# Optimization experiments

Hardware: AMD Instinct MI355X
Metric: run time of the kernel (lower is better)

The kernel has to match this reference:

```python
import jax, jax.numpy as jnp
import numpy as np

TEMPERATURE = 0.07
NEG = -1e9  # stand-in for -inf on the diagonal; exp(NEG) == 0


def setup_inputs() -> dict:
    key = jax.random.key(0)
    k1, k2, k3 = jax.random.split(key, 3)
    B, D = 4096, 1024
    return {
        "anchor_features": jax.random.normal(k1, (B, D), dtype=jnp.float32),
        "positive_features": jax.random.normal(k2, (B, D), dtype=jnp.float32),
        "labels": jax.random.randint(k3, (B,), 0, 2),
    }


def reference(anchor_features, positive_features, labels):
    B = anchor_features.shape[0]
    # L2-normalize (normalize=True)
    a = anchor_features / jnp.linalg.norm(anchor_features, axis=1, keepdims=True)
    p = positive_features / jnp.linalg.norm(positive_features, axis=1, keepdims=True)
    feats = jnp.concatenate([a, p], axis=0)                      # [2B, D]
    sim = jnp.matmul(feats, feats.T) / TEMPERATURE               # [2B, 2B]
    diag = jnp.eye(2 * B, dtype=bool)
    sim = jnp.where(diag, NEG, sim)                              # mask self-similarity
    # logsumexp over all non-self entries per row (diag contributes exp(NEG)=0)
    lse = jax.nn.logsumexp(sim, axis=1)                          # [2B]
    # positive pair similarity: sim[i, i+B] == sim[i+B, i] == <a_i, p_i>/t
    cross = jnp.sum(a * p, axis=1) / TEMPERATURE                 # [B]
    pos_sim = jnp.concatenate([cross, cross])                    # [2B]
    lab = jnp.concatenate([labels, labels]).astype(sim.dtype)    # [2B], 0/1
    per_row = (-pos_sim + lse) * lab
    num_pos = jnp.sum(lab)
    return jnp.where(num_pos > 0, jnp.sum(per_row) / num_pos, jnp.float32(0.0))
```

## Files before the change

### kernel.cpp

```cpp
#include <hip/hip_runtime.h>
#include <hip/hip_bf16.h>

#define TEMP_INV (1.0f / 0.07f)
#define LOG2E 1.4426950408889634f
#define LN2 0.6931471805599453f
#define CFIX 21.0f

typedef __attribute__((ext_vector_type(4))) float f32x4;

__device__ __forceinline__ void gload16(const unsigned char* g,
                                        unsigned char* l) {
  __builtin_amdgcn_global_load_lds(
      (const __attribute__((address_space(1))) void*)g,
      (__attribute__((address_space(3))) void*)l, 16, 0, 0);
}

__global__ __launch_bounds__(256) void norm_kernel(
    const float* __restrict__ A, const float* __restrict__ P,
    unsigned char* __restrict__ F, float* __restrict__ cross,
    float* __restrict__ lsum, int B, int D) {
  const int row = blockIdx.x;
  const int t = threadIdx.x;
  {
    const int zi = row * 256 + t;
    if (zi < 2 * B) lsum[zi] = 0.f;
  }
  const float4* a4 = reinterpret_cast<const float4*>(A + (size_t)row * D);
  const float4* p4 = reinterpret_cast<const float4*>(P + (size_t)row * D);
  const int n4 = D >> 2;
  float sa = 0.f, sp = 0.f, sx = 0.f;
  for (int i = t; i < n4; i += 256) {
    float4 av = a4[i], pv = p4[i];
    sa += av.x * av.x + av.y * av.y + av.z * av.z + av.w * av.w;
    sp += pv.x * pv.x + pv.y * pv.y + pv.z * pv.z + pv.w * pv.w;
    sx += av.x * pv.x + av.y * pv.y + av.z * pv.z + av.w * pv.w;
  }
#pragma unroll
  for (int off = 32; off; off >>= 1) {
    sa += __shfl_down(sa, off);
    sp += __shfl_down(sp, off);
    sx += __shfl_down(sx, off);
  }
  __shared__ float red[3][4];
  const int wid = t >> 6, lane = t & 63;
  if (lane == 0) { red[0][wid] = sa; red[1][wid] = sp; red[2][wid] = sx; }
  __syncthreads();
  sa = red[0][0] + red[0][1] + red[0][2] + red[0][3];
  sp = red[1][0] + red[1][1] + red[1][2] + red[1][3];
  sx = red[2][0] + red[2][1] + red[2][2] + red[2][3];
  const float ian = rsqrtf(sa), ipn = rsqrtf(sp);
  const float ia = ian * 16.f, ip = ipn * 16.f;
  unsigned char* fa = F + (size_t)row * D;
  unsigned char* fp = F + (size_t)(B + row) * D;
  for (int i = t; i < n4; i += 256) {
    float4 av = a4[i], pv = p4[i];
    int qa = 0, qp = 0;
    qa = __builtin_amdgcn_cvt_pk_fp8_f32(av.x * ia, av.y * ia, qa, false);
    qa = __builtin_amdgcn_cvt_pk_fp8_f32(av.z * ia, av.w * ia, qa, true);
    qp = __builtin_amdgcn_cvt_pk_fp8_f32(pv.x * ip, pv.y * ip, qp, false);
    qp = __builtin_amdgcn_cvt_pk_fp8_f32(pv.z * ip, pv.w * ip, qp, true);
    reinterpret_cast<int*>(fa)[i] = qa;
    reinterpret_cast<int*>(fp)[i] = qp;
  }
  if (t == 0) cross[row] = sx * ian * ipn;
}

#define VT 16

__global__ __launch_bounds__(512, 2) void gram_lse_kernel(
    const unsigned char* __restrict__ F, float* __restrict__ lsum, int NN,
    int D) {
  __shared__ unsigned char lds8[4][2][2][8192];
  const int nrb = NN >> 8;
  const int ntri = nrb * (nrb + 1) / 2;
  int b = blockIdx.x;
  b = (b & 7) * (gridDim.x >> 3) + (b >> 3);
  const int lin0 = b * 3;

  const int t = threadIdx.x;
  const int lane = t & 63, w = t >> 6;
  const int lo = lane & 15, hi = lane >> 4;
  const int wr = w >> 2, wn = w & 3;

  const int ci = t;
  const int lrS = ci >> 3, cuS = (ci & 7) ^ (lrS & 7);
  const int trowS = lrS * 4 + (cuS >> 1), kcS = (cuS & 1) << 4;
  const int dstW = w * 1024;

  int offA[8], offB[4];
#pragma unroll
  for (int mf = 0; mf < 8; ++mf) {
    const int r = wr * 128 + mf * 16 + lo;
    const int lr = r >> 2;
    const int cu = ((r & 3) << 1) | (hi >> 1);
    offA[mf] = lr * 128 + ((cu ^ (lr & 7)) << 4) + ((hi & 1) << 3);
  }
#pragma unroll
  for (int nf = 0; nf < 4; ++nf) {
    const int r = wn * 64 + nf * 16 + lo;
    const int lr = r >> 2;
    const int cu = ((r & 3) << 1) | (hi >> 1);
    offB[nf] = lr * 128 + ((cu ^ (lr & 7)) << 4) + ((hi & 1) << 3);
  }

  const float scl = LOG2E * TEMP_INV / 256.f;

  for (int ti = 0; ti < 3; ++ti) {
    const int lin = lin0 + ti;
    int by = (int)((sqrtf(8.f * (float)lin + 1.f) - 1.f) * 0.5f);
    while ((by + 1) * (by + 2) / 2 <= lin) ++by;
    while (by * (by + 1) / 2 > lin) --by;
    const int bx = lin - by * (by + 1) / 2;
    const int r0 = bx * 256;
    const int c0 = by * 256;
    const bool diag = (bx == by);

    const unsigned char* srcA = F + (size_t)(c0 + trowS) * D + kcS;
    const unsigned char* srcB = F + (size_t)(r0 + trowS) * D + kcS;

#define STAGE_A(T, KS)                                              \
  do {                                                              \
    int v_ = (T); if (v_ > VT - 1) v_ = VT - 1;                     \
    gload16(srcA + v_ * 64 + (KS) * 32, &lds8[(T) & 3][0][KS][dstW]); \
  } while (0)
#define STAGE_B(T, KS)                                              \
  do {                                                              \
    int v_ = (T); if (v_ > VT - 1) v_ = VT - 1;                     \
    gload16(srcB + v_ * 64 + (KS) * 32, &lds8[(T) & 3][1][KS][dstW]); \
  } while (0)

    f32x4 acc[8][4];
#pragma unroll
    for (int a = 0; a < 8; ++a)
#pragma unroll
      for (int bb = 0; bb < 4; ++bb) acc[a][bb] = (f32x4){0.f, 0.f, 0.f, 0.f};

#pragma unroll
    for (int pt = 0; pt < 3; ++pt) {
      STAGE_A(pt, 0); STAGE_B(pt, 0);
      STAGE_A(pt, 1); STAGE_B(pt, 1);
    }

    for (int v = 0; v < VT; ++v) {
      const int buf = v & 3;
      asm volatile("s_waitcnt vmcnt(8)" ::: "memory");
      __builtin_amdgcn_s_barrier();
      asm volatile("" ::: "memory");

#pragma unroll
      for (int KS = 0; KS < 2; ++KS) {
        const unsigned char* RA = &lds8[buf][0][KS][0];
        const unsigned char* RB = &lds8[buf][1][KS][0];
        long aF[8], bF[4];
#pragma unroll
        for (int nf = 0; nf < 4; ++nf) bF[nf] = *(const long*)(RB + offB[nf]);
#pragma unroll
        for (int mf = 0; mf < 8; ++mf) aF[mf] = *(const long*)(RA + offA[mf]);

        if (KS == 0) { STAGE_A(v + 3, 0); STAGE_B(v + 3, 0); }
        else         { STAGE_A(v + 3, 1); STAGE_B(v + 3, 1); }

        __builtin_amdgcn_s_setprio(1);
#pragma unroll
        for (int mf = 0; mf < 8; ++mf)
#pragma unroll
          for (int nf = 0; nf < 4; ++nf)
            acc[mf][nf] = __builtin_amdgcn_mfma_f32_16x16x32_fp8_fp8(
                aF[mf], bF[nf], acc[mf][nf], 0, 0, 0);
        __builtin_amdgcn_s_setprio(0);
      }
      asm volatile("" ::: "memory");
    }

    float s_i[4] = {0.f, 0.f, 0.f, 0.f};
    float s_j[32];
#pragma unroll
    for (int q = 0; q < 32; ++q) s_j[q] = 0.f;
    {
      const int jb2 = c0 + wr * 128;
#pragma unroll
      for (int nf = 0; nf < 4; ++nf) {
        const int dg = (r0 + wn * 64 + nf * 16 + lo) - jb2;
#pragma unroll
        for (int mf = 0; mf < 8; ++mf)
#pragma unroll
          for (int rg = 0; rg < 4; ++rg) {
            const int jloc = mf * 16 + hi * 4 + rg;
            float e = exp2f(acc[mf][nf][rg] * scl - CFIX);
            if (diag && dg == jloc) e = 0.f;
            s_i[nf] += e;
            s_j[mf * 4 + rg] += e;
          }
      }
    }
#pragma unroll
    for (int nf = 0; nf < 4; ++nf) {
      float v = s_i[nf];
      v += __shfl_xor(v, 16);
      v += __shfl_xor(v, 32);
      if (hi == 0) atomicAdd(&lsum[r0 + wn * 64 + nf * 16 + lo], v);
    }
    if (!diag) {
#pragma unroll
      for (int q = 0; q < 32; ++q) {
        float v = s_j[q];
        v += __shfl_xor(v, 1);
        v += __shfl_xor(v, 2);
        v += __shfl_xor(v, 4);
        v += __shfl_xor(v, 8);
        if (lo == 0)
          atomicAdd(&lsum[c0 + wr * 128 + (q >> 2) * 16 + hi * 4 + (q & 3)],
                    v);
      }
    }

    asm volatile("s_waitcnt vmcnt(0)" ::: "memory");
    __builtin_amdgcn_s_barrier();
    asm volatile("" ::: "memory");
#undef STAGE_A
#undef STAGE_B
  }
}

__global__ __launch_bounds__(256) void finalize_part(
    const float* __restrict__ lsum, const float* __restrict__ cross,
    const int* __restrict__ labels, float* __restrict__ bsum,
    float* __restrict__ bcnt, int B) {
  const int NN = 2 * B;
  const int i = blockIdx.x * 256 + threadIdx.x;
  float sum = 0.f, cnt = 0.f;
  if (i < NN) {
    const float lse = LN2 * (CFIX + log2f(lsum[i]));
    const float lab = (float)labels[i % B];
    sum = (lse - cross[i % B] * TEMP_INV) * lab;
    cnt = lab;
  }
#pragma unroll
  for (int off = 32; off; off >>= 1) {
    sum += __shfl_down(sum, off);
    cnt += __shfl_down(cnt, off);
  }
  __shared__ float rs[4], rc[4];
  const int wid = threadIdx.x >> 6, lane = threadIdx.x & 63;
  if (lane == 0) { rs[wid] = sum; rc[wid] = cnt; }
  __syncthreads();
  if (threadIdx.x == 0) {
    bsum[blockIdx.x] = rs[0] + rs[1] + rs[2] + rs[3];
    bcnt[blockIdx.x] = rc[0] + rc[1] + rc[2] + rc[3];
  }
}

__global__ __launch_bounds__(64) void finalize_final(
    const float* __restrict__ bsum, const float* __restrict__ bcnt,
    float* __restrict__ out, int nb) {
  const int t = threadIdx.x;
  float s = (t < nb) ? bsum[t] : 0.f;
  float c = (t < nb) ? bcnt[t] : 0.f;
#pragma unroll
  for (int off = 32; off; off >>= 1) {
    s += __shfl_down(s, off);
    c += __shfl_down(c, off);
  }
  if (t == 0) out[0] = (c > 0.f) ? s / c : 0.f;
}

extern "C" void kernel_launch(void* const* d_in, const int* in_sizes, int n_in,
                              void* d_out, int out_size, void* d_ws, size_t ws_size,
                              hipStream_t stream) {
  const float* A = (const float*)d_in[0];
  const float* P = (const float*)d_in[1];
  const int* labels = (const int*)d_in[2];
  float* out = (float*)d_out;
  const int B = in_sizes[2];
  const int D = in_sizes[0] / B;
  const int NN = 2 * B;

  char* ws = (char*)d_ws;
  unsigned char* F = (unsigned char*)ws;
  size_t off = (size_t)NN * D;
  off = (off + 255) & ~(size_t)255;
  float* cross = (float*)(ws + off);
  off += (size_t)B * sizeof(float);
  off = (off + 255) & ~(size_t)255;
  float* lsum = (float*)(ws + off);
  off += (size_t)NN * sizeof(float);
  off = (off + 255) & ~(size_t)255;
  float* bsum = (float*)(ws + off);
  off += 64 * sizeof(float);
  float* bcnt = (float*)(ws + off);

  norm_kernel<<<B, 256, 0, stream>>>(A, P, F, cross, lsum, B, D);
  const int nrb = NN >> 8;
  const int ntri = nrb * (nrb + 1) / 2;
  gram_lse_kernel<<<ntri / 3, 512, 0, stream>>>(F, lsum, NN, D);
  const int nb = (NN + 255) / 256;
  finalize_part<<<nb, 256, 0, stream>>>(lsum, cross, labels, bsum, bcnt, B);
  finalize_final<<<1, 64, 0, stream>>>(bsum, bcnt, out, nb);
}
```

Before: 115.4 us.

## Prefetch next tile's first K-steps across tile boundary and merge finalize kernels

Inside the persistent gram kernel, each block processes three triangular tiles. Previously the tail prefetches were clamped, redundant loads of the last K-slice, and every tile restarted its pipeline prologue. Now the tail stages load the first slices of the next tile, so the prologue runs only for the first tile and the pipeline stays filled across tile boundaries. The two finalize kernels are also merged into one 1024-thread single-block kernel to save a launch. This relies on the LDS ring-buffer indexing staying consistent across tiles, and the final reduction now runs in a single block.

```diff
diff --git a/kernel.cpp b/kernel.cpp
--- a/kernel.cpp
+++ b/kernel.cpp
@@ -118,15 +118,25 @@
     const unsigned char* srcA = F + (size_t)(c0 + trowS) * D + kcS;
     const unsigned char* srcB = F + (size_t)(r0 + trowS) * D + kcS;
 
-#define STAGE_A(T, KS)                                              \
-  do {                                                              \
-    int v_ = (T); if (v_ > VT - 1) v_ = VT - 1;                     \
-    gload16(srcA + v_ * 64 + (KS) * 32, &lds8[(T) & 3][0][KS][dstW]); \
+    const int linN = (ti < 2) ? (lin + 1) : lin;
+    int byN = (int)((sqrtf(8.f * (float)linN + 1.f) - 1.f) * 0.5f);
+    while ((byN + 1) * (byN + 2) / 2 <= linN) ++byN;
+    while (byN * (byN + 1) / 2 > linN) --byN;
+    const int bxN = linN - byN * (byN + 1) / 2;
+    const unsigned char* srcA2 = F + (size_t)(byN * 256 + trowS) * D + kcS;
+    const unsigned char* srcB2 = F + (size_t)(bxN * 256 + trowS) * D + kcS;
+
+#define STAGE_A(T, KS)                                                    \
+  do {                                                                    \
+    const unsigned char* pa_ =                                            \
+        ((T) < VT) ? (srcA + (T) * 64) : (srcA2 + ((T) - VT) * 64);       \
+    gload16(pa_ + (KS) * 32, &lds8[(T) & 3][0][KS][dstW]);                \
   } while (0)
-#define STAGE_B(T, KS)                                              \
-  do {                                                              \
-    int v_ = (T); if (v_ > VT - 1) v_ = VT - 1;                     \
-    gload16(srcB + v_ * 64 + (KS) * 32, &lds8[(T) & 3][1][KS][dstW]); \
+#define STAGE_B(T, KS)                                                    \
+  do {                                                                    \
+    const unsigned char* pb_ =                                            \
+        ((T) < VT) ? (srcB + (T) * 64) : (srcB2 + ((T) - VT) * 64);       \
+    gload16(pb_ + (KS) * 32, &lds8[(T) & 3][1][KS][dstW]);                \
   } while (0)
 
     f32x4 acc[8][4];
@@ -135,10 +145,12 @@
 #pragma unroll
       for (int bb = 0; bb < 4; ++bb) acc[a][bb] = (f32x4){0.f, 0.f, 0.f, 0.f};
 
-#pragma unroll
-    for (int pt = 0; pt < 3; ++pt) {
-      STAGE_A(pt, 0); STAGE_B(pt, 0);
-      STAGE_A(pt, 1); STAGE_B(pt, 1);
+    if (ti == 0) {
+#pragma unroll
+      for (int pt = 0; pt < 3; ++pt) {
+        STAGE_A(pt, 0); STAGE_B(pt, 0);
+        STAGE_A(pt, 1); STAGE_B(pt, 1);
+      }
     }
 
     for (int v = 0; v < VT; ++v) {
@@ -222,46 +234,32 @@
   }
 }
 
-__global__ __launch_bounds__(256) void finalize_part(
+__global__ __launch_bounds__(1024) void finalize_kernel(
     const float* __restrict__ lsum, const float* __restrict__ cross,
-    const int* __restrict__ labels, float* __restrict__ bsum,
-    float* __restrict__ bcnt, int B) {
+    const int* __restrict__ labels, float* __restrict__ out, int B) {
   const int NN = 2 * B;
-  const int i = blockIdx.x * 256 + threadIdx.x;
+  const int t = threadIdx.x;
   float sum = 0.f, cnt = 0.f;
-  if (i < NN) {
+  for (int i = t; i < NN; i += 1024) {
     const float lse = LN2 * (CFIX + log2f(lsum[i]));
     const float lab = (float)labels[i % B];
-    sum = (lse - cross[i % B] * TEMP_INV) * lab;
-    cnt = lab;
+    sum += (lse - cross[i % B] * TEMP_INV) * lab;
+    cnt += lab;
   }
 #pragma unroll
   for (int off = 32; off; off >>= 1) {
     sum += __shfl_down(sum, off);
     cnt += __shfl_down(cnt, off);
   }
-  __shared__ float rs[4], rc[4];
-  const int wid = threadIdx.x >> 6, lane = threadIdx.x & 63;
+  __shared__ float rs[16], rc[16];
+  const int wid = t >> 6, lane = t & 63;
   if (lane == 0) { rs[wid] = sum; rc[wid] = cnt; }
   __syncthreads();
-  if (threadIdx.x == 0) {
-    bsum[blockIdx.x] = rs[0] + rs[1] + rs[2] + rs[3];
-    bcnt[blockIdx.x] = rc[0] + rc[1] + rc[2] + rc[3];
-  }
-}
-
-__global__ __launch_bounds__(64) void finalize_final(
-    const float* __restrict__ bsum, const float* __restrict__ bcnt,
-    float* __restrict__ out, int nb) {
-  const int t = threadIdx.x;
-  float s = (t < nb) ? bsum[t] : 0.f;
-  float c = (t < nb) ? bcnt[t] : 0.f;
-#pragma unroll
-  for (int off = 32; off; off >>= 1) {
-    s += __shfl_down(s, off);
-    c += __shfl_down(c, off);
-  }
-  if (t == 0) out[0] = (c > 0.f) ? s / c : 0.f;
+  if (t == 0) {
+    float S = 0.f, C = 0.f;
+    for (int q = 0; q < 16; ++q) { S += rs[q]; C += rc[q]; }
+    out[0] = (C > 0.f) ? S / C : 0.f;
+  }
 }
 
 extern "C" void kernel_launch(void* const* d_in, const int* in_sizes, int n_in,
@@ -283,17 +281,10 @@
   off += (size_t)B * sizeof(float);
   off = (off + 255) & ~(size_t)255;
   float* lsum = (float*)(ws + off);
-  off += (size_t)NN * sizeof(float);
-  off = (off + 255) & ~(size_t)255;
-  float* bsum = (float*)(ws + off);
-  off += 64 * sizeof(float);
-  float* bcnt = (float*)(ws + off);
 
   norm_kernel<<<B, 256, 0, stream>>>(A, P, F, cross, lsum, B, D);
   const int nrb = NN >> 8;
   const int ntri = nrb * (nrb + 1) / 2;
   gram_lse_kernel<<<ntri / 3, 512, 0, stream>>>(F, lsum, NN, D);
-  const int nb = (NN + 255) / 256;
-  finalize_part<<<nb, 256, 0, stream>>>(lsum, cross, labels, bsum, bcnt, B);
-  finalize_final<<<1, 64, 0, stream>>>(bsum, bcnt, out, nb);
-}
+  finalize_kernel<<<1, 1024, 0, stream>>>(lsum, cross, labels, out, B);
+}
```

After: 115.7 us. Within noise of the previous version (+0.3%).
